# Kernel optimization log

Measured on AMD Instinct MI355X. Metric: run time of the kernel, lower is better.

## Reference

```python
import jax, jax.numpy as jnp
import numpy as np

B, L, DC, DD, A = 32, 1024, 1024, 1024, 1024
NEG = -1e10


def setup_inputs() -> dict:
    key = jax.random.key(0)
    ks = jax.random.split(key, 16)
    s = lambda fan_in: 1.0 / np.sqrt(fan_in)
    return {
        "caption_features": jax.random.normal(ks[0], (B, L, DC), jnp.float32),
        "decoder_hidden": jax.random.normal(ks[1], (B, DD), jnp.float32),
        "word": jax.random.normal(ks[2], (B, DC), jnp.float32),
        "prev_caption_mask": jax.random.randint(ks[3], (B, L), 0, 2, jnp.int32),
        # cap_features_att: Linear(DC, A)
        "Wf": jax.random.uniform(ks[4], (A, DC), jnp.float32, -s(DC), s(DC)),
        "bf": jax.random.uniform(ks[5], (A,), jnp.float32, -s(DC), s(DC)),
        # cap_decoder_att: Linear(DD, A)
        "Wd": jax.random.uniform(ks[6], (A, DD), jnp.float32, -s(DD), s(DD)),
        "bd": jax.random.uniform(ks[7], (A,), jnp.float32, -s(DD), s(DD)),
        # cap_full_att: Linear(A, 1)
        "Wa": jax.random.uniform(ks[8], (1, A), jnp.float32, -s(A), s(A)),
        "ba": jax.random.uniform(ks[9], (1,), jnp.float32, -s(A), s(A)),
        # context_gate: Linear(2*DC + DD, DC)
        "Wg": jax.random.uniform(ks[10], (DC, 2 * DC + DD), jnp.float32, -s(2 * DC + DD), s(2 * DC + DD)),
        "bg": jax.random.uniform(ks[11], (DC,), jnp.float32, -s(2 * DC + DD), s(2 * DC + DD)),
        # sc_affine: Linear(DC, DC)
        "Ws": jax.random.uniform(ks[12], (DC, DC), jnp.float32, -s(DC), s(DC)),
        "bs": jax.random.uniform(ks[13], (DC,), jnp.float32, -s(DC), s(DC)),
        # tc_affine: Linear(2*DD, DC)
        "Wt": jax.random.uniform(ks[14], (DC, 2 * DD), jnp.float32, -s(2 * DD), s(2 * DD)),
        "bt": jax.random.uniform(ks[15], (DC,), jnp.float32, -s(2 * DD), s(2 * DD)),
    }


def reference(caption_features, decoder_hidden, word, prev_caption_mask,
              Wf, bf, Wd, bd, Wa, ba, Wg, bg, Ws, bs, Wt, bt):
    # additive (Bahdanau) attention scores: (B, L)
    att1 = jnp.einsum('bld,ad->bla', caption_features, Wf) + bf          # (B, L, A)
    att2 = decoder_hidden @ Wd.T + bd                                    # (B, A)
    scores = jnp.einsum('bla,a->bl', jnp.tanh(att1 + att2[:, None, :]), Wa[0]) + ba[0]
    scores = jnp.where(prev_caption_mask == 0, NEG, scores)
    alpha = jax.nn.softmax(scores, axis=1)                               # (B, L)
    context = jnp.einsum('bl,bld->bd', alpha, caption_features)          # (B, DC)
    # gated fusion
    zt = jax.nn.sigmoid(jnp.concatenate([word, decoder_hidden, context], axis=1) @ Wg.T + bg)
    sc = jnp.tanh(context @ Ws.T + bs)
    tc = jnp.tanh(jnp.concatenate([word, decoder_hidden], axis=1) @ Wt.T + bt)
    gated_context = zt * sc + (1.0 - zt) * tc
    return (gated_context, alpha)
```

## Files before the change

kernel.cpp:

```cpp
#include <hip/hip_runtime.h>
#include <hip/hip_bf16.h>
#include <cstdint>
#include <cstddef>

#define LOG2E 1.4426950408889634f

typedef __attribute__((ext_vector_type(8))) short short8;
typedef __attribute__((ext_vector_type(4))) float f32x4;

__device__ __forceinline__ float exp2f_fast(float x) { return __builtin_amdgcn_exp2f(x); }
__device__ __forceinline__ float rcp_fast(float x)   { return __builtin_amdgcn_rcpf(x); }
__device__ __forceinline__ float tanh_fast(float x) {
  float e = exp2f_fast(x * (2.0f * LOG2E));
  return 1.0f - 2.0f * rcp_fast(e + 1.0f);
}
__device__ __forceinline__ unsigned short f2b(float f) {
  union { float f; unsigned int u; } v; v.f = f;
  return (unsigned short)((v.u + 0x7FFFu + ((v.u >> 16) & 1u)) >> 16);
}
__device__ __forceinline__ float b2f(short h) {
  union { unsigned u; float f; } w; w.u = ((unsigned)(unsigned short)h) << 16;
  return w.f;
}

#define GLOAD_LDS16(g, l) \
  __builtin_amdgcn_global_load_lds((const __attribute__((address_space(1))) unsigned int*)(g), \
                                   (__attribute__((address_space(3))) unsigned int*)(l), 16, 0, 0)

__device__ __forceinline__ void skinny_gemm(
    const float* __restrict__ W, int Kfull,
    const float* __restrict__ x0, const float* __restrict__ x1,
    const float* __restrict__ x2,
    int kbeg, int kend, int n0, float* __restrict__ out)
{
  __shared__ unsigned char sX[4096];
  const int tid = threadIdx.x, lane = tid & 63, wv = tid >> 6;
  const int l15 = lane & 15, l4 = lane >> 4;
  f32x4 acc[2][2];
#pragma unroll
  for (int m = 0; m < 2; ++m)
#pragma unroll
    for (int j = 0; j < 2; ++j) acc[m][j] = (f32x4){0.f, 0.f, 0.f, 0.f};

  const int srow = tid >> 3, skc = (tid & 7) * 8;
  const int sbyte = srow * 128 + ((skc * 2) ^ ((srow & 7) << 4));

  for (int k0 = kbeg; k0 < kend; k0 += 64) {
    const float* xs = (k0 < 1024) ? x0 : (k0 < 2048) ? x1 : x2;
    const float* xp = xs + srow * 1024 + (k0 & 1023) + skc;
    float4 a = *reinterpret_cast<const float4*>(xp);
    float4 b = *reinterpret_cast<const float4*>(xp + 4);
    short8 h;
    h[0] = (short)f2b(a.x); h[1] = (short)f2b(a.y); h[2] = (short)f2b(a.z); h[3] = (short)f2b(a.w);
    h[4] = (short)f2b(b.x); h[5] = (short)f2b(b.y); h[6] = (short)f2b(b.z); h[7] = (short)f2b(b.w);
    *reinterpret_cast<short8*>(sX + sbyte) = h;
    __syncthreads();
#pragma unroll
    for (int ks = 0; ks < 2; ++ks) {
      short8 af[2], bfr[2];
#pragma unroll
      for (int m = 0; m < 2; ++m) {
        int r = m * 16 + l15;
        af[m] = *reinterpret_cast<const short8*>(
            sX + r * 128 + (((ks * 64) + l4 * 16) ^ ((r & 7) << 4)));
      }
#pragma unroll
      for (int j = 0; j < 2; ++j) {
        int n = n0 + wv * 32 + j * 16 + l15;
        const float* wp = W + (size_t)n * Kfull + k0 + ks * 32 + l4 * 8;
        float4 wa = *reinterpret_cast<const float4*>(wp);
        float4 wb = *reinterpret_cast<const float4*>(wp + 4);
        short8 hb;
        hb[0] = (short)f2b(wa.x); hb[1] = (short)f2b(wa.y); hb[2] = (short)f2b(wa.z); hb[3] = (short)f2b(wa.w);
        hb[4] = (short)f2b(wb.x); hb[5] = (short)f2b(wb.y); hb[6] = (short)f2b(wb.z); hb[7] = (short)f2b(wb.w);
        bfr[j] = hb;
      }
#pragma unroll
      for (int m = 0; m < 2; ++m)
#pragma unroll
        for (int j = 0; j < 2; ++j)
          acc[m][j] = __builtin_amdgcn_mfma_f32_16x16x32_bf16(af[m], bfr[j], acc[m][j], 0, 0, 0);
    }
    __syncthreads();
  }
#pragma unroll
  for (int m = 0; m < 2; ++m)
#pragma unroll
    for (int j = 0; j < 2; ++j)
#pragma unroll
      for (int r = 0; r < 4; ++r)
        atomicAdd(out + (size_t)(m * 16 + l4 * 4 + r) * 1024 + (n0 + wv * 32 + j * 16 + l15),
                  acc[m][j][r]);
}

__global__ __launch_bounds__(256) void convert_att2(
    const float* __restrict__ wf, unsigned short* __restrict__ wfb,
    const float* __restrict__ Wd, const float* __restrict__ dh,
    float* __restrict__ att2)
{
  const int bid = blockIdx.x;
  if (bid < 128) {
    const int base = bid * 1024;
#pragma unroll
    for (int j = 0; j < 4; ++j) {
      int g = base + j * 256 + (int)threadIdx.x;
      const float* s = wf + (size_t)g * 8;
      float4 a = *reinterpret_cast<const float4*>(s);
      float4 b = *reinterpret_cast<const float4*>(s + 4);
      short8 o;
      o[0] = (short)f2b(a.x); o[1] = (short)f2b(a.y); o[2] = (short)f2b(a.z); o[3] = (short)f2b(a.w);
      o[4] = (short)f2b(b.x); o[5] = (short)f2b(b.y); o[6] = (short)f2b(b.z); o[7] = (short)f2b(b.w);
      *reinterpret_cast<short8*>(wfb + (size_t)g * 8) = o;
    }
  } else {
    int bid2 = bid - 128;
    int nt = bid2 & 7, ks = bid2 >> 3;
    skinny_gemm(Wd, 1024, dh, dh, dh, ks * 512, ks * 512 + 512, nt * 128, att2);
  }
}

__global__ __launch_bounds__(256) void gate_gemm(
    const float* __restrict__ Wg, const float* __restrict__ Ws_,
    const float* __restrict__ Wt, const float* __restrict__ word,
    const float* __restrict__ dh, const float* __restrict__ ctx,
    float* __restrict__ ztp, float* __restrict__ scp, float* __restrict__ tcp)
{
  const int nt = blockIdx.x, slot = blockIdx.y;
  if (slot < 6)
    skinny_gemm(Wg, 3072, word, dh, ctx, slot * 512, slot * 512 + 512, nt * 128, ztp);
  else if (slot < 8)
    skinny_gemm(Ws_, 1024, ctx, ctx, ctx, (slot - 6) * 512, (slot - 6) * 512 + 512, nt * 128, scp);
  else
    skinny_gemm(Wt, 2048, word, dh, dh, (slot - 8) * 512, (slot - 8) * 512 + 512, nt * 128, tcp);
}

__global__ __launch_bounds__(512, 2) void att_gemm3(
    const float* __restrict__ cap, const unsigned short* __restrict__ wfb,
    const float* __restrict__ att2pre, const float* __restrict__ bfv,
    const float* __restrict__ bdv, const float* __restrict__ Wa,
    float* __restrict__ scores)
{
  __shared__ __align__(16) unsigned char lds[131072];
  const int tid = threadIdx.x, lane = tid & 63, wv = tid >> 6;
  const int j = ((int)blockIdx.x & 7) * 64 + ((int)blockIdx.x >> 3);
  const int mt = j >> 2, nt = j & 3;
  const int m0 = mt << 8, n0 = nt << 8;
  const int bb = m0 >> 10;
  const int wm = wv >> 2, wn = wv & 3;
  const int l15 = lane & 15, l4 = lane >> 4;
  const int r8 = lane >> 3, c8 = lane & 7;
  const unsigned swb = (unsigned)((l15 & 7) << 4);

  const float* capA = cap + (size_t)(m0 + wv * 32 + r8) * 1024 +
                      ((unsigned)((c8 * 16) ^ (r8 << 4)) >> 1);
  const unsigned char* bSrc = (const unsigned char*)wfb +
      (size_t)(n0 + wv * 32 + r8) * 2048 + ((c8 * 16) ^ (r8 << 4));
  const unsigned ldsBase = (unsigned)(size_t)(&lds[0]);

  f32x4 acc[8][4];
#pragma unroll
  for (int mf = 0; mf < 8; ++mf)
#pragma unroll
    for (int nf = 0; nf < 4; ++nf) acc[mf][nf] = (f32x4){0.f, 0.f, 0.f, 0.f};

#define STAGE_B(t) do { \
    const int sl__ = (t) & 1; \
    unsigned char* db__ = lds + sl__ * 65536 + 32768 + wv * 4096; \
    const unsigned char* gb__ = bSrc + (t) * 128; \
    GLOAD_LDS16(gb__,          db__); \
    GLOAD_LDS16(gb__ + 16384,  db__ + 1024); \
    GLOAD_LDS16(gb__ + 32768,  db__ + 2048); \
    GLOAD_LDS16(gb__ + 49152,  db__ + 3072); \
  } while (0)

#define FLIGHT(fA0, fA1, fB0, fB1, j0, tt) do { \
    const float* p0__ = capA + (size_t)(j0) * 8192 + (tt) * 64; \
    const float* p1__ = p0__ + 8192; \
    fA0 = *reinterpret_cast<const float4*>(p0__); \
    fA1 = *reinterpret_cast<const float4*>(p0__ + 4); \
    fB0 = *reinterpret_cast<const float4*>(p1__); \
    fB1 = *reinterpret_cast<const float4*>(p1__ + 4); \
  } while (0)

#define PACK_WRITE(fA, fB, wp) do { \
    short8 o__; \
    o__[0] = (short)f2b(fA.x); o__[1] = (short)f2b(fA.y); \
    o__[2] = (short)f2b(fA.z); o__[3] = (short)f2b(fA.w); \
    o__[4] = (short)f2b(fB.x); o__[5] = (short)f2b(fB.y); \
    o__[6] = (short)f2b(fB.z); o__[7] = (short)f2b(fB.w); \
    *reinterpret_cast<short8*>(wp) = o__; \
  } while (0)

#define DSREAD(dst, addr) \
  asm volatile("ds_read_b128 %0, %1" : "=v"(dst) : "v"(addr))

#define READ_AQ(dst, q) do { \
_Pragma("unroll") \
    for (int mf2 = 0; mf2 < 2; ++mf2) \
_Pragma("unroll") \
      for (int ks = 0; ks < 2; ++ks) { \
        unsigned r__ = (unsigned)(wm * 128 + (q) * 32 + mf2 * 16 + l15); \
        DSREAD(dst[mf2 * 2 + ks], sA + r__ * 128 + (((unsigned)(ks * 64 + l4 * 16)) ^ swb)); \
      } \
  } while (0)

#define READ_B(ch) do { \
_Pragma("unroll") \
    for (int nf = 0; nf < 2; ++nf) \
_Pragma("unroll") \
      for (int ks = 0; ks < 2; ++ks) { \
        unsigned c__ = (unsigned)(wn * 64 + (ch) * 32 + nf * 16 + l15); \
        DSREAD(Breg[(ch) * 4 + nf * 2 + ks], sB + c__ * 128 + (((unsigned)(ks * 64 + l4 * 16)) ^ swb)); \
      } \
  } while (0)

#define MFMA8(q, ch, Aq) do { \
    __builtin_amdgcn_s_setprio(1); \
_Pragma("unroll") \
    for (int mf2 = 0; mf2 < 2; ++mf2) \
_Pragma("unroll") \
      for (int nf = 0; nf < 2; ++nf) \
_Pragma("unroll") \
        for (int ks = 0; ks < 2; ++ks) \
          acc[(q) * 2 + mf2][(ch) * 2 + nf] = __builtin_amdgcn_mfma_f32_16x16x32_bf16( \
              Aq[mf2 * 2 + ks], Breg[(ch) * 4 + nf * 2 + ks], acc[(q) * 2 + mf2][(ch) * 2 + nf], 0, 0, 0); \
    __builtin_amdgcn_s_setprio(0); \
  } while (0)

#define WAIT_LGKM(n) do { \
    asm volatile("s_waitcnt lgkmcnt(" #n ")" ::: "memory"); \
    __builtin_amdgcn_sched_barrier(0); \
  } while (0)

  short8 Aq0[4], Aq1[4], Breg[8];
  float4 g0a, g0b, g1a, g1b;
  float4 g2a, g2b, g3a, g3b;

  STAGE_B(0);
  FLIGHT(g0a, g0b, g1a, g1b, 0, 0);
  FLIGHT(g2a, g2b, g3a, g3b, 2, 0);
  asm volatile("s_waitcnt vmcnt(0)" ::: "memory");
  {
    unsigned char* wp = lds + wv * 4096 + lane * 16;
    PACK_WRITE(g0a, g0b, wp);
    PACK_WRITE(g1a, g1b, wp + 1024);
    PACK_WRITE(g2a, g2b, wp + 2048);
    PACK_WRITE(g3a, g3b, wp + 3072);
  }
  FLIGHT(g0a, g0b, g1a, g1b, 0, 1);
  FLIGHT(g2a, g2b, g3a, g3b, 2, 1);
  WAIT_LGKM(0);
  asm volatile("s_barrier" ::: "memory");

  for (int t = 0; t < 16; ++t) {
    const unsigned sA = ldsBase + (unsigned)((t & 1) * 65536);
    const unsigned sB = sA + 32768u;

    if (t < 15) {
      asm volatile("s_waitcnt vmcnt(0)" ::: "memory");
      __builtin_amdgcn_sched_barrier(0);
      unsigned char* wp = lds + ((t + 1) & 1) * 65536 + wv * 4096 + lane * 16;
      PACK_WRITE(g0a, g0b, wp);
      PACK_WRITE(g1a, g1b, wp + 1024);
      PACK_WRITE(g2a, g2b, wp + 2048);
      PACK_WRITE(g3a, g3b, wp + 3072);
    }
    if (t < 15) STAGE_B(t + 1);

    READ_AQ(Aq0, 0);
    READ_B(0);
    READ_B(1);
    READ_AQ(Aq1, 1);

    WAIT_LGKM(8);
    MFMA8(0, 0, Aq0);
    WAIT_LGKM(4);
    MFMA8(0, 1, Aq0);
    WAIT_LGKM(0);
    READ_AQ(Aq0, 2);
    MFMA8(1, 0, Aq1);
    MFMA8(1, 1, Aq1);
    READ_AQ(Aq1, 3);
    WAIT_LGKM(4);
    MFMA8(2, 0, Aq0);
    MFMA8(2, 1, Aq0);
    if (t < 14) FLIGHT(g0a, g0b, g1a, g1b, 0, t + 2);
    WAIT_LGKM(0);
    MFMA8(3, 0, Aq1);
    MFMA8(3, 1, Aq1);
    if (t < 14) FLIGHT(g2a, g2b, g3a, g3b, 2, t + 2);

    if (t < 15) {
      if (t < 14) {
        asm volatile("s_waitcnt vmcnt(8)" ::: "memory");
      } else {
        asm volatile("s_waitcnt vmcnt(0)" ::: "memory");
      }
      asm volatile("s_barrier" ::: "memory");
    }
  }

  float colb[4], wav[4];
#pragma unroll
  for (int nf = 0; nf < 4; ++nf) {
    int cg = n0 + wn * 64 + nf * 16 + l15;
    colb[nf] = att2pre[bb * 1024 + cg] + bfv[cg] + bdv[cg];
    wav[nf]  = Wa[cg];
  }
#pragma unroll
  for (int mf = 0; mf < 8; ++mf) {
#pragma unroll
    for (int r = 0; r < 4; ++r) {
      float s = tanh_fast(acc[mf][0][r] + colb[0]) * wav[0]
              + tanh_fast(acc[mf][1][r] + colb[1]) * wav[1]
              + tanh_fast(acc[mf][2][r] + colb[2]) * wav[2]
              + tanh_fast(acc[mf][3][r] + colb[3]) * wav[3];
      s += __shfl_xor(s, 1);
      s += __shfl_xor(s, 2);
      s += __shfl_xor(s, 4);
      s += __shfl_xor(s, 8);
      if (l15 == 0)
        atomicAdd(scores + (m0 + wm * 128 + mf * 16 + l4 * 4 + r), s);
    }
  }
#undef STAGE_B
#undef FLIGHT
#undef PACK_WRITE
#undef DSREAD
#undef READ_AQ
#undef READ_B
#undef MFMA8
#undef WAIT_LGKM
}

__global__ __launch_bounds__(256) void softmax_k(
    const float* __restrict__ scores, const int* __restrict__ mask,
    float* __restrict__ alpha)
{
  const int b = blockIdx.x, tid = threadIdx.x;
  __shared__ float red[8];
  float s[4];
  float mx = -3.0e38f;
#pragma unroll
  for (int i = 0; i < 4; ++i) {
    int l = tid + i * 256;
    float v = scores[b * 1024 + l];
    v = (mask[b * 1024 + l] == 0) ? -1.0e10f : v;
    s[i] = v;
    mx = fmaxf(mx, v);
  }
  for (int off = 1; off < 64; off <<= 1) mx = fmaxf(mx, __shfl_xor(mx, off));
  int wv = tid >> 6;
  if ((tid & 63) == 0) red[wv] = mx;
  __syncthreads();
  mx = fmaxf(fmaxf(red[0], red[1]), fmaxf(red[2], red[3]));
  float sum = 0.f;
#pragma unroll
  for (int i = 0; i < 4; ++i) {
    s[i] = exp2f_fast((s[i] - mx) * LOG2E);
    sum += s[i];
  }
  for (int off = 1; off < 64; off <<= 1) sum += __shfl_xor(sum, off);
  if ((tid & 63) == 0) red[4 + wv] = sum;
  __syncthreads();
  sum = red[4] + red[5] + red[6] + red[7];
  float inv = 1.0f / sum;
#pragma unroll
  for (int i = 0; i < 4; ++i) alpha[b * 1024 + tid + i * 256] = s[i] * inv;
}

__global__ __launch_bounds__(256) void ctx_kb(
    const float* __restrict__ cap, const float* __restrict__ alpha,
    float* __restrict__ ctx)
{
  const int b = blockIdx.y, lc = blockIdx.x;
  const int dc = threadIdx.x & 127, loff = threadIdx.x >> 7;
  float acc[8] = {0.f, 0.f, 0.f, 0.f, 0.f, 0.f, 0.f, 0.f};
  for (int l = lc * 128 + loff; l < lc * 128 + 128; l += 2) {
    float av = alpha[b * 1024 + l];
    if (av != 0.f) {
      const float* p = cap + (((size_t)(b * 1024 + l)) << 10) + dc * 8;
      float4 v0 = *reinterpret_cast<const float4*>(p);
      float4 v1 = *reinterpret_cast<const float4*>(p + 4);
      acc[0] += av * v0.x; acc[1] += av * v0.y;
      acc[2] += av * v0.z; acc[3] += av * v0.w;
      acc[4] += av * v1.x; acc[5] += av * v1.y;
      acc[6] += av * v1.z; acc[7] += av * v1.w;
    }
  }
#pragma unroll
  for (int j = 0; j < 8; ++j) atomicAdd(ctx + b * 1024 + dc * 8 + j, acc[j]);
}

__global__ __launch_bounds__(256) void final_k(
    const float* __restrict__ ztp, const float* __restrict__ scp,
    const float* __restrict__ tcp, const float* __restrict__ bg,
    const float* __restrict__ bs, const float* __restrict__ bt,
    float* __restrict__ out)
{
  const int idx = blockIdx.x * 256 + threadIdx.x;
  const int d = idx & 1023;
  float z  = rcp_fast(1.0f + exp2f_fast(-(ztp[idx] + bg[d]) * LOG2E));
  float sc = tanh_fast(scp[idx] + bs[d]);
  float tc = tanh_fast(tcp[idx] + bt[d]);
  out[idx] = z * sc + (1.0f - z) * tc;
}

extern "C" void kernel_launch(void* const* d_in, const int* in_sizes, int n_in,
                              void* d_out, int out_size, void* d_ws, size_t ws_size,
                              hipStream_t stream) {
  const float* cap  = (const float*)d_in[0];
  const float* dh   = (const float*)d_in[1];
  const float* word = (const float*)d_in[2];
  const int*   mask = (const int*)d_in[3];
  const float* Wf   = (const float*)d_in[4];
  const float* bf   = (const float*)d_in[5];
  const float* Wd   = (const float*)d_in[6];
  const float* bd   = (const float*)d_in[7];
  const float* Wa   = (const float*)d_in[8];
  const float* Wg   = (const float*)d_in[10];
  const float* bg   = (const float*)d_in[11];
  const float* Ws   = (const float*)d_in[12];
  const float* bs   = (const float*)d_in[13];
  const float* Wt   = (const float*)d_in[14];
  const float* bt   = (const float*)d_in[15];

  float* out_g = (float*)d_out;
  float* alpha = (float*)d_out + 32768;

  float* att2pre = (float*)d_ws;
  float* scores  = att2pre + 32768;
  float* ctx     = scores + 32768;
  float* ztp     = ctx + 32768;
  float* scp     = ztp + 32768;
  float* tcp     = scp + 32768;
  unsigned short* wfb = (unsigned short*)((char*)d_ws + 786432);

  hipMemsetAsync(d_ws, 0, 6 * 32768 * sizeof(float), stream);

  convert_att2<<<144, 256, 0, stream>>>(Wf, wfb, Wd, dh, att2pre);
  att_gemm3<<<512, 512, 0, stream>>>(cap, wfb, att2pre, bf, bd, Wa, scores);
  softmax_k<<<32, 256, 0, stream>>>(scores, mask, alpha);
  ctx_kb<<<dim3(8, 32), 256, 0, stream>>>(cap, alpha, ctx);
  gate_gemm<<<dim3(8, 12), 256, 0, stream>>>(Wg, Ws, Wt, word, dh, ctx, ztp, scp, tcp);
  final_k<<<128, 256, 0, stream>>>(ztp, scp, tcp, bg, bs, bt, out_g);
}
```

Measured before the change: 156.3 us.

## Compact unmasked rows and skip attention GEMM work on masked positions

```diff
diff --git a/kernel.cpp b/kernel.cpp
--- a/kernel.cpp
+++ b/kernel.cpp
@@ -91,6 +91,41 @@
       for (int r = 0; r < 4; ++r)
         atomicAdd(out + (size_t)(m * 16 + l4 * 4 + r) * 1024 + (n0 + wv * 32 + j * 16 + l15),
                   acc[m][j][r]);
+}
+
+__global__ __launch_bounds__(1024) void compact_k(
+    const int* __restrict__ mask, int* __restrict__ liveIdx,
+    int* __restrict__ meta)
+{
+  __shared__ int cnt[1024];
+  __shared__ int sDead;
+  const int tid = threadIdx.x;
+  if (tid == 0) sDead = 0x7fffffff;
+  __syncthreads();
+  const int base = tid * 32;
+  int c = 0, firstDead = 0x7fffffff;
+  for (int i = 0; i < 32; ++i) {
+    int m = mask[base + i];
+    if (m != 0) ++c;
+    else if (firstDead == 0x7fffffff) firstDead = base + i;
+  }
+  if (firstDead != 0x7fffffff) atomicMin(&sDead, firstDead);
+  cnt[tid] = c;
+  __syncthreads();
+  for (int off = 1; off < 1024; off <<= 1) {
+    int v = cnt[tid];
+    int a = (tid >= off) ? cnt[tid - off] : 0;
+    __syncthreads();
+    cnt[tid] = v + a;
+    __syncthreads();
+  }
+  int woff = cnt[tid] - c;
+  for (int i = 0; i < 32; ++i) {
+    int r = base + i;
+    if (mask[r] != 0) liveIdx[woff++] = r;
+  }
+  __syncthreads();
+  if (tid == 1023) { meta[0] = cnt[1023]; meta[1] = sDead; }
 }
 
 __global__ __launch_bounds__(256) void convert_att2(
@@ -138,6 +173,7 @@
     const float* __restrict__ cap, const unsigned short* __restrict__ wfb,
     const float* __restrict__ att2pre, const float* __restrict__ bfv,
     const float* __restrict__ bdv, const float* __restrict__ Wa,
+    const int* __restrict__ liveIdx, const int* __restrict__ meta,
     float* __restrict__ scores)
 {
   __shared__ __align__(16) unsigned char lds[131072];
@@ -145,14 +181,23 @@
   const int j = ((int)blockIdx.x & 7) * 64 + ((int)blockIdx.x >> 3);
   const int mt = j >> 2, nt = j & 3;
   const int m0 = mt << 8, n0 = nt << 8;
-  const int bb = m0 >> 10;
+  const int nLive = meta[0];
+  const int nLiveR = (nLive + 255) & ~255;
+  if (m0 >= nLiveR) return;
+  const int deadIdx = meta[1];
   const int wm = wv >> 2, wn = wv & 3;
   const int l15 = lane & 15, l4 = lane >> 4;
   const int r8 = lane >> 3, c8 = lane & 7;
   const unsigned swb = (unsigned)((l15 & 7) << 4);
 
-  const float* capA = cap + (size_t)(m0 + wv * 32 + r8) * 1024 +
-                      ((unsigned)((c8 * 16) ^ (r8 << 4)) >> 1);
+  const unsigned swzf32 = ((unsigned)((c8 * 16) ^ (r8 << 4)) >> 1);
+  unsigned rOff[4];
+#pragma unroll
+  for (int c = 0; c < 4; ++c) {
+    int cr = m0 + wv * 32 + c * 8 + r8;
+    int orow = (cr < nLive) ? liveIdx[cr] : deadIdx;
+    rOff[c] = ((unsigned)orow << 10) + swzf32;
+  }
   const unsigned char* bSrc = (const unsigned char*)wfb +
       (size_t)(n0 + wv * 32 + r8) * 2048 + ((c8 * 16) ^ (r8 << 4));
   const unsigned ldsBase = (unsigned)(size_t)(&lds[0]);
@@ -174,8 +219,8 @@
   } while (0)
 
 #define FLIGHT(fA0, fA1, fB0, fB1, j0, tt) do { \
-    const float* p0__ = capA + (size_t)(j0) * 8192 + (tt) * 64; \
-    const float* p1__ = p0__ + 8192; \
+    const float* p0__ = cap + rOff[j0] + (tt) * 64; \
+    const float* p1__ = cap + rOff[(j0) + 1] + (tt) * 64; \
     fA0 = *reinterpret_cast<const float4*>(p0__); \
     fA1 = *reinterpret_cast<const float4*>(p0__ + 4); \
     fB0 = *reinterpret_cast<const float4*>(p1__); \
@@ -300,27 +345,31 @@
     }
   }
 
-  float colb[4], wav[4];
+  float wav[4], cb0[4];
 #pragma unroll
   for (int nf = 0; nf < 4; ++nf) {
     int cg = n0 + wn * 64 + nf * 16 + l15;
-    colb[nf] = att2pre[bb * 1024 + cg] + bfv[cg] + bdv[cg];
-    wav[nf]  = Wa[cg];
-  }
+    cb0[nf] = bfv[cg] + bdv[cg];
+    wav[nf] = Wa[cg];
+  }
+  const int cgBase = n0 + wn * 64 + l15;
 #pragma unroll
   for (int mf = 0; mf < 8; ++mf) {
 #pragma unroll
     for (int r = 0; r < 4; ++r) {
-      float s = tanh_fast(acc[mf][0][r] + colb[0]) * wav[0]
-              + tanh_fast(acc[mf][1][r] + colb[1]) * wav[1]
-              + tanh_fast(acc[mf][2][r] + colb[2]) * wav[2]
-              + tanh_fast(acc[mf][3][r] + colb[3]) * wav[3];
+      int grow = m0 + wm * 128 + mf * 16 + l4 * 4 + r;
+      int orow = (grow < nLive) ? liveIdx[grow] : deadIdx;
+      const float* a2 = att2pre + ((orow >> 10) << 10) + cgBase;
+      float s = tanh_fast(acc[mf][0][r] + a2[0]  + cb0[0]) * wav[0]
+              + tanh_fast(acc[mf][1][r] + a2[16] + cb0[1]) * wav[1]
+              + tanh_fast(acc[mf][2][r] + a2[32] + cb0[2]) * wav[2]
+              + tanh_fast(acc[mf][3][r] + a2[48] + cb0[3]) * wav[3];
       s += __shfl_xor(s, 1);
       s += __shfl_xor(s, 2);
       s += __shfl_xor(s, 4);
       s += __shfl_xor(s, 8);
       if (l15 == 0)
-        atomicAdd(scores + (m0 + wm * 128 + mf * 16 + l4 * 4 + r), s);
+        atomicAdd(scores + orow, s);
     }
   }
 #undef STAGE_B
@@ -435,11 +484,15 @@
   float* scp     = ztp + 32768;
   float* tcp     = scp + 32768;
   unsigned short* wfb = (unsigned short*)((char*)d_ws + 786432);
+  int* liveIdx = (int*)((char*)d_ws + 786432 + 2097152);
+  int* meta    = (int*)((char*)d_ws + 786432 + 2097152 + 131072);
 
   hipMemsetAsync(d_ws, 0, 6 * 32768 * sizeof(float), stream);
 
+  compact_k<<<1, 1024, 0, stream>>>(mask, liveIdx, meta);
   convert_att2<<<144, 256, 0, stream>>>(Wf, wfb, Wd, dh, att2pre);
-  att_gemm3<<<512, 512, 0, stream>>>(cap, wfb, att2pre, bf, bd, Wa, scores);
+  att_gemm3<<<512, 512, 0, stream>>>(cap, wfb, att2pre, bf, bd, Wa,
+                                     liveIdx, meta, scores);
   softmax_k<<<32, 256, 0, stream>>>(scores, mask, alpha);
   ctx_kb<<<dim3(8, 32), 256, 0, stream>>>(cap, alpha, ctx);
   gate_gemm<<<dim3(8, 12), 256, 0, stream>>>(Wg, Ws, Wt, word, dh, ctx, ztp, scp, tcp);
```

Result: slower. 213.7 us (+36.7%).
